# Kernel optimization log

Hardware: AMD Instinct MI355X
Metric: run time of the kernel (lower is better)

## Reference

```python
import jax, jax.numpy as jnp
import numpy as np

N = 100000      # nodes
E = 3200000     # edges
IN_DIM = 128
HID = 128
OUT_DIM = 1
LAYERS = 8
ALPHA = 0.1
THETA = 0.5


def setup_inputs() -> dict:
    key = jax.random.key(0)
    ks = jax.random.split(key, 8)
    x = jax.random.normal(ks[0], (N, IN_DIM), dtype=jnp.float32)
    edge_index = jax.random.randint(ks[1], (2, E), 0, N, dtype=jnp.int64)
    edge_weight = jax.random.uniform(ks[2], (E,), dtype=jnp.float32)  # unused by original forward path
    W_in = jax.random.normal(ks[3], (IN_DIM, HID), dtype=jnp.float32) * 0.05
    b_in = jnp.zeros((HID,), dtype=jnp.float32)
    W_gcn = jax.random.normal(ks[4], (LAYERS, HID, HID), dtype=jnp.float32) * 0.05
    W_out = jax.random.normal(ks[5], (HID, OUT_DIM), dtype=jnp.float32) * 0.05
    b_out = jnp.zeros((OUT_DIM,), dtype=jnp.float32)
    return {"x": x, "edge_weight": edge_weight, "W_in": W_in, "b_in": b_in,
            "W_gcn": W_gcn, "W_out": W_out, "b_out": b_out, "edge_index": edge_index}


def _gcn_norm(edge_index, dtype):
    # add self loops (fill value 1), symmetric normalization deg^-1/2 A deg^-1/2
    sl = jnp.arange(N, dtype=edge_index.dtype)
    row = jnp.concatenate([edge_index[0], sl])
    col = jnp.concatenate([edge_index[1], sl])
    w = jnp.ones(row.shape[0], dtype=dtype)
    deg = jax.ops.segment_sum(w, col, num_segments=N)
    dinv = jnp.where(deg > 0, jax.lax.rsqrt(deg), 0.0)
    norm = dinv[row] * dinv[col]
    return row, col, norm


def reference(x, edge_weight, W_in, b_in, W_gcn, W_out, b_out, edge_index):
    row, col, norm = _gcn_norm(edge_index, x.dtype)
    h = x @ W_in + b_in            # initial_proj
    h0 = h                          # residual x0
    for i in range(LAYERS):
        # dropout is identity in eval mode
        msg = h[row] * norm[:, None]                       # gather + scale [E+N, HID]
        agg = jax.ops.segment_sum(msg, col, num_segments=N)
        s = (1.0 - ALPHA) * agg + ALPHA * h0               # identity-mapped residual
        beta = float(np.log(THETA / (i + 1) + 1.0))
        h = (1.0 - beta) * s + beta * (s @ W_gcn[i])       # GCNII weight mix
        h = jax.nn.relu(h)
    return h @ W_out + b_out
```

## Files before the change

kernel.cpp:

```cpp
#include <hip/hip_runtime.h>
#include <hip/hip_bf16.h>
#include <math.h>

#define N_NODES 100000
#define N_EDGES 3200000
#define HID 128
#define LAYERS 8
#define ALPHA 0.1f
#define THETA 0.5f

#define SH 8
#define NODES8 (N_NODES * SH)
#define SCAN_TILE 4096
#define NB_SCAN ((NODES8 + SCAN_TILE - 1) / SCAN_TILE)

typedef unsigned int uint;
typedef unsigned short ushort;
typedef __attribute__((ext_vector_type(8))) short short8;
typedef __attribute__((ext_vector_type(4))) float f32x4;

__device__ inline float bf_lo(uint p) { return __uint_as_float(p << 16); }
__device__ inline float bf_hi(uint p) { return __uint_as_float(p & 0xffff0000u); }
__device__ inline uint bf_pack(float x, float y) {
    uint ux = __float_as_uint(x), uy = __float_as_uint(y);
    uint rx = (ux + 0x7fffu + ((ux >> 16) & 1u)) >> 16;
    uint ry = (uy + 0x7fffu + ((uy >> 16) & 1u)) >> 16;
    return rx | (ry << 16);
}
__device__ inline ushort bfr(float x) {
    uint u = __float_as_uint(x);
    return (ushort)((u + 0x7fffu + ((u >> 16) & 1u)) >> 16);
}
__device__ inline float bff(ushort s) { return __uint_as_float(((uint)s) << 16); }

__global__ __launch_bounds__(256) void k_count(const int* __restrict__ col,
                                               int* __restrict__ cnt8) {
    int e = blockIdx.x * 256 + threadIdx.x;
    int shard = blockIdx.x & (SH - 1);
    if (e < N_EDGES) atomicAdd(&cnt8[col[e] * SH + shard], 1);
}

__global__ __launch_bounds__(256) void k_dinv(const int* __restrict__ cnt8,
                                              float* __restrict__ dinv) {
    int n = blockIdx.x * 256 + threadIdx.x;
    if (n >= N_NODES) return;
    int4 a = *(const int4*)(cnt8 + n * SH);
    int4 b = *(const int4*)(cnt8 + n * SH + 4);
    int deg = a.x + a.y + a.z + a.w + b.x + b.y + b.z + b.w;
    dinv[n] = rsqrtf((float)(deg + 1));
}

__global__ __launch_bounds__(256) void k_scan1(const int* __restrict__ cnt8,
                                               int* __restrict__ indptr8,
                                               int* __restrict__ bsum) {
    __shared__ int lds[256];
    int t = threadIdx.x;
    int base = blockIdx.x * SCAN_TILE + t * 16;
    int v[16];
    int s = 0;
#pragma unroll
    for (int j = 0; j < 16; ++j) {
        v[j] = (base + j < NODES8) ? cnt8[base + j] : 0;
        s += v[j];
    }
    lds[t] = s;
    __syncthreads();
    for (int off = 1; off < 256; off <<= 1) {
        int u = (t >= off) ? lds[t - off] : 0;
        __syncthreads();
        lds[t] += u;
        __syncthreads();
    }
    int run = lds[t] - s;
#pragma unroll
    for (int j = 0; j < 16; ++j) {
        if (base + j < NODES8) indptr8[base + j] = run;
        run += v[j];
    }
    if (t == 255) bsum[blockIdx.x] = lds[255];
}

__global__ __launch_bounds__(256) void k_scan2(const int* __restrict__ bsum,
                                               int* __restrict__ boff) {
    __shared__ int lds[256];
    int t = threadIdx.x;
    int v = (t < NB_SCAN) ? bsum[t] : 0;
    lds[t] = v;
    __syncthreads();
    for (int off = 1; off < 256; off <<= 1) {
        int u = (t >= off) ? lds[t - off] : 0;
        __syncthreads();
        lds[t] += u;
        __syncthreads();
    }
    boff[t] = lds[t] - v;
}

__global__ __launch_bounds__(256) void k_scan3(int* __restrict__ indptr8,
                                               const int* __restrict__ boff) {
    int base = blockIdx.x * SCAN_TILE + threadIdx.x * 16;
    int add = boff[blockIdx.x];
#pragma unroll
    for (int j = 0; j < 16; ++j) {
        if (base + j < NODES8) indptr8[base + j] += add;
    }
    if (blockIdx.x == 0 && threadIdx.x == 0) indptr8[NODES8] = N_EDGES;
}

__global__ __launch_bounds__(256) void k_fill(const int* __restrict__ rowi,
                                              const int* __restrict__ coli,
                                              const float* __restrict__ dinv,
                                              const int* __restrict__ indptr8,
                                              int* __restrict__ cursor8,
                                              int2* __restrict__ csr) {
    int e = blockIdx.x * 256 + threadIdx.x;
    if (e >= N_EDGES) return;
    int shard = blockIdx.x & (SH - 1);
    int r = rowi[e];
    int c = coli[e];
    int slot = c * SH + shard;
    int p = indptr8[slot] + atomicAdd(&cursor8[slot], 1);
    csr[p] = make_int2(r, __float_as_int(dinv[r] * dinv[c]));
}

__global__ __launch_bounds__(256) void k_wprep(const float* __restrict__ Wg,
                                               ushort* __restrict__ Wt) {
    int l = blockIdx.x;
    const float* W = Wg + (size_t)l * HID * HID;
    ushort* T = Wt + (size_t)l * HID * HID;
    int t = threadIdx.x;
#pragma unroll
    for (int i = 0; i < 16; ++i) {
        int idx = t + 256 * i;
        int k = idx >> 5;
        int c4 = idx & 31;
        float4 v = *(const float4*)(W + (size_t)k * HID + c4 * 4);
        T[(c4 * 4 + 0) * HID + k] = bfr(v.x);
        T[(c4 * 4 + 1) * HID + k] = bfr(v.y);
        T[(c4 * 4 + 2) * HID + k] = bfr(v.z);
        T[(c4 * 4 + 3) * HID + k] = bfr(v.w);
    }
}

__global__ __launch_bounds__(256) void k_spmm(const uint* __restrict__ h,
                                              const uint* __restrict__ h0,
                                              const float* __restrict__ dinv,
                                              const int* __restrict__ indptr8,
                                              const int2* __restrict__ csr,
                                              uint* __restrict__ s_out) {
    int node = blockIdx.x * 4 + (threadIdx.x >> 6);
    if (node >= N_NODES) return;
    int lane = threadIdx.x & 63;
    int beg = indptr8[node * SH];
    int end = indptr8[node * SH + SH];
    float di = dinv[node];
    uint hs = h[node * 64 + lane];
    uint h0v = h0[node * 64 + lane];
    float ax[8], ay[8];
#pragma unroll
    for (int j = 0; j < 8; ++j) { ax[j] = 0.f; ay[j] = 0.f; }
    int e = beg;
    for (; e + 16 <= end; e += 16) {
        int2 rr[16];
#pragma unroll
        for (int j = 0; j < 16; ++j) rr[j] = csr[e + j];
        uint p[16];
#pragma unroll
        for (int j = 0; j < 16; ++j) p[j] = h[rr[j].x * 64 + lane];
#pragma unroll
        for (int j = 0; j < 16; ++j) {
            float w = __int_as_float(rr[j].y);
            ax[j & 7] = fmaf(w, bf_lo(p[j]), ax[j & 7]);
            ay[j & 7] = fmaf(w, bf_hi(p[j]), ay[j & 7]);
        }
    }
    for (; e < end; e += 4) {
        int2 rr[4];
        float w[4];
#pragma unroll
        for (int j = 0; j < 4; ++j) {
            int idx = e + j;
            rr[j] = csr[idx < end ? idx : beg];
            w[j] = (idx < end) ? __int_as_float(rr[j].y) : 0.f;
        }
        uint p[4];
#pragma unroll
        for (int j = 0; j < 4; ++j) p[j] = h[rr[j].x * 64 + lane];
#pragma unroll
        for (int j = 0; j < 4; ++j) {
            ax[j] = fmaf(w[j], bf_lo(p[j]), ax[j]);
            ay[j] = fmaf(w[j], bf_hi(p[j]), ay[j]);
        }
    }
    float sum0 = ((ax[0] + ax[1]) + (ax[2] + ax[3])) + ((ax[4] + ax[5]) + (ax[6] + ax[7]));
    float sum1 = ((ay[0] + ay[1]) + (ay[2] + ay[3])) + ((ay[4] + ay[5]) + (ay[6] + ay[7]));
    float selfw = di * di;
    float rx = (1.0f - ALPHA) * fmaf(selfw, bf_lo(hs), sum0) + ALPHA * bf_lo(h0v);
    float ry = (1.0f - ALPHA) * fmaf(selfw, bf_hi(hs), sum1) + ALPHA * bf_hi(h0v);
    s_out[node * 64 + lane] = bf_pack(rx, ry);
}

__global__ __launch_bounds__(256) void k_gemm_in(const float* __restrict__ A,
                                                 const float* __restrict__ W,
                                                 const float* __restrict__ bias,
                                                 uint* __restrict__ out0,
                                                 uint* __restrict__ out1) {
    __shared__ float sT[32 * 64];
    __shared__ float Ws[32 * 128];
    int t = threadIdx.x;
    int tr = t & 15;
    int tc = t >> 4;
    int rowBase = blockIdx.x * 64;
    float acc[4][8] = {};

    for (int ko = 0; ko < HID; ko += 32) {
#pragma unroll
        for (int pass = 0; pass < 2; ++pass) {
            int lin = t + 256 * pass;
            int r = lin >> 3;
            int kq = lin & 7;
            int ar = rowBase + r;
            if (ar >= N_NODES) ar = N_NODES - 1;
            float4 v = *(const float4*)(A + (size_t)ar * HID + ko + 4 * kq);
            sT[(4 * kq + 0) * 64 + r] = v.x;
            sT[(4 * kq + 1) * 64 + r] = v.y;
            sT[(4 * kq + 2) * 64 + r] = v.z;
            sT[(4 * kq + 3) * 64 + r] = v.w;
        }
#pragma unroll
        for (int pass = 0; pass < 4; ++pass) {
            int lin = t + 256 * pass;
            int k = lin >> 5;
            int c4 = lin & 31;
            *(float4*)&Ws[k * 128 + 4 * c4] =
                *(const float4*)(W + (size_t)(ko + k) * HID + 4 * c4);
        }
        __syncthreads();
#pragma unroll
        for (int k = 0; k < 32; ++k) {
            float4 a = *(const float4*)&sT[k * 64 + 4 * tr];
            float4 w0 = *(const float4*)&Ws[k * 128 + 8 * tc];
            float4 w1 = *(const float4*)&Ws[k * 128 + 8 * tc + 4];
            float av[4] = {a.x, a.y, a.z, a.w};
            float wv[8] = {w0.x, w0.y, w0.z, w0.w, w1.x, w1.y, w1.z, w1.w};
#pragma unroll
            for (int i = 0; i < 4; ++i)
#pragma unroll
                for (int j = 0; j < 8; ++j)
                    acc[i][j] = fmaf(av[i], wv[j], acc[i][j]);
        }
        __syncthreads();
    }

    int c0 = 8 * tc;
    float bb[8];
#pragma unroll
    for (int j = 0; j < 8; ++j) bb[j] = bias[c0 + j];
#pragma unroll
    for (int i = 0; i < 4; ++i) {
        int r = rowBase + 4 * tr + i;
        if (r >= N_NODES) break;
        float v[8];
#pragma unroll
        for (int j = 0; j < 8; ++j) v[j] = acc[i][j] + bb[j];
        uint4 o;
        o.x = bf_pack(v[0], v[1]);
        o.y = bf_pack(v[2], v[3]);
        o.z = bf_pack(v[4], v[5]);
        o.w = bf_pack(v[6], v[7]);
        *(uint4*)(out0 + (size_t)r * 64 + c0 / 2) = o;
        *(uint4*)(out1 + (size_t)r * 64 + c0 / 2) = o;
    }
}

#define SAS 136

__global__ __launch_bounds__(256) void k_gemm_layer(const uint* __restrict__ A,
                                                    const ushort* __restrict__ Wt,
                                                    uint* __restrict__ out0,
                                                    float beta) {
    __shared__ ushort sA[64 * SAS];
    __shared__ ushort sW[128 * SAS];
    int t = threadIdx.x;
    int lane = t & 63;
    int wv = t >> 6;
    int rowBase = blockIdx.x * 64;

#pragma unroll
    for (int i = 0; i < 4; ++i) {
        int idx = t + 256 * i;
        int r = idx >> 4;
        int q = idx & 15;
        int ar = rowBase + r;
        if (ar >= N_NODES) ar = N_NODES - 1;
        uint4 v = *(const uint4*)(A + (size_t)ar * 64 + q * 4);
        *(uint4*)((uint*)(sA + r * SAS) + q * 4) = v;
    }
#pragma unroll
    for (int i = 0; i < 8; ++i) {
        int idx = t + 256 * i;
        int r = idx >> 4;
        int q = idx & 15;
        uint4 v = *(const uint4*)((const uint*)(Wt + (size_t)r * HID) + q * 4);
        *(uint4*)((uint*)(sW + r * SAS) + q * 4) = v;
    }
    __syncthreads();

    int fr = lane & 15;
    int fq = lane >> 4;
    f32x4 acc[4][2] = {};
#pragma unroll
    for (int kc = 0; kc < 4; ++kc) {
        int kof = kc * 32 + fq * 8;
        short8 b0 = *(const short8*)(sW + (wv * 32 + fr) * SAS + kof);
        short8 b1 = *(const short8*)(sW + (wv * 32 + 16 + fr) * SAS + kof);
#pragma unroll
        for (int tm = 0; tm < 4; ++tm) {
            short8 a = *(const short8*)(sA + (tm * 16 + fr) * SAS + kof);
            acc[tm][0] = __builtin_amdgcn_mfma_f32_16x16x32_bf16(a, b0, acc[tm][0], 0, 0, 0);
            acc[tm][1] = __builtin_amdgcn_mfma_f32_16x16x32_bf16(a, b1, acc[tm][1], 0, 0, 0);
        }
    }
    __syncthreads();

    ushort* pack = sW;
    float ob = 1.0f - beta;
#pragma unroll
    for (int tm = 0; tm < 4; ++tm)
#pragma unroll
        for (int tn = 0; tn < 2; ++tn)
#pragma unroll
            for (int r = 0; r < 4; ++r) {
                int row = tm * 16 + fq * 4 + r;
                int col = wv * 32 + tn * 16 + fr;
                float sv = bff(sA[row * SAS + col]);
                float val = fmaxf(fmaf(ob, sv, beta * acc[tm][tn][r]), 0.f);
                pack[row * 128 + col] = bfr(val);
            }
    __syncthreads();
#pragma unroll
    for (int i = 0; i < 4; ++i) {
        int idx = t + 256 * i;
        int r = idx >> 4;
        int q = idx & 15;
        int ar = rowBase + r;
        if (ar < N_NODES)
            *(uint4*)(out0 + (size_t)ar * 64 + q * 4) =
                *(const uint4*)((const uint*)(pack + r * 128) + q * 4);
    }
}

__global__ __launch_bounds__(256) void k_out(const uint* __restrict__ h,
                                             const float* __restrict__ W_out,
                                             const float* __restrict__ b_out,
                                             float* __restrict__ out) {
    int node = blockIdx.x * 4 + (threadIdx.x >> 6);
    if (node >= N_NODES) return;
    int lane = threadIdx.x & 63;
    uint p = h[node * 64 + lane];
    float2 wv = *(const float2*)(W_out + lane * 2);
    float pr = bf_lo(p) * wv.x + bf_hi(p) * wv.y;
#pragma unroll
    for (int off = 32; off > 0; off >>= 1) pr += __shfl_down(pr, off);
    if (lane == 0) out[node] = pr + b_out[0];
}

extern "C" void kernel_launch(void* const* d_in, const int* in_sizes, int n_in,
                              void* d_out, int out_size, void* d_ws, size_t ws_size,
                              hipStream_t stream) {
    const float* x     = (const float*)d_in[0];
    const float* W_in  = (const float*)d_in[2];
    const float* b_in  = (const float*)d_in[3];
    const float* W_gcn = (const float*)d_in[4];
    const float* W_out = (const float*)d_in[5];
    const float* b_out = (const float*)d_in[6];
    const int*   ei    = (const int*)d_in[7];
    const int* rowi = ei;
    const int* coli = ei + N_EDGES;
    float* out = (float*)d_out;

    char* ws = (char*)d_ws;
    auto alloc = [&](size_t bytes) -> char* {
        char* p = ws;
        ws += (bytes + 255) & ~(size_t)255;
        return p;
    };
    int*    cnt8    = (int*)   alloc((size_t)NODES8 * 4);
    float*  dinv    = (float*) alloc((size_t)N_NODES * 4);
    int*    indptr8 = (int*)   alloc((size_t)(NODES8 + 8) * 4);
    int*    cursor8 = (int*)   alloc((size_t)NODES8 * 4);
    int*    bsum    = (int*)   alloc(1024 * 4);
    int*    boff    = (int*)   alloc(1024 * 4);
    int2*   csr     = (int2*)  alloc((size_t)N_EDGES * 8);
    ushort* Wt      = (ushort*)alloc((size_t)LAYERS * HID * HID * 2);
    uint*   hA      = (uint*)  alloc((size_t)N_NODES * 64 * 4);
    uint*   hB      = (uint*)  alloc((size_t)N_NODES * 64 * 4);
    uint*   h0      = (uint*)  alloc((size_t)N_NODES * 64 * 4);

    hipMemsetAsync(cnt8, 0, (size_t)NODES8 * 4, stream);
    hipMemsetAsync(cursor8, 0, (size_t)NODES8 * 4, stream);

    k_count<<<(N_EDGES + 255) / 256, 256, 0, stream>>>(coli, cnt8);
    k_dinv<<<(N_NODES + 255) / 256, 256, 0, stream>>>(cnt8, dinv);
    k_scan1<<<NB_SCAN, 256, 0, stream>>>(cnt8, indptr8, bsum);
    k_scan2<<<1, 256, 0, stream>>>(bsum, boff);
    k_scan3<<<NB_SCAN, 256, 0, stream>>>(indptr8, boff);
    k_fill<<<(N_EDGES + 255) / 256, 256, 0, stream>>>(rowi, coli, dinv, indptr8,
                                                      cursor8, csr);
    k_wprep<<<LAYERS, 256, 0, stream>>>(W_gcn, Wt);

    int gemm_blocks = (N_NODES + 63) / 64;
    k_gemm_in<<<gemm_blocks, 256, 0, stream>>>(x, W_in, b_in, h0, hA);

    for (int l = 0; l < LAYERS; ++l) {
        k_spmm<<<(N_NODES + 3) / 4, 256, 0, stream>>>(hA, h0, dinv, indptr8,
                                                      csr, hB);
        float beta = logf(THETA / (float)(l + 1) + 1.0f);
        k_gemm_layer<<<gemm_blocks, 256, 0, stream>>>(
            hB, Wt + (size_t)l * HID * HID, hA, beta);
    }
    k_out<<<(N_NODES + 3) / 4, 256, 0, stream>>>(hA, W_out, b_out, out);
}
```

Baseline: 1.533 ms.

## Build CSR via two-pass bucket binning with source-chunk sorted shards

Replaces the single atomic scatter CSR fill with a two-pass build: edges are first binned into 64-node destination buckets through coarse global atomics, then each bucket is scattered into CSR using shared-memory cursors. Shards are now keyed by source-node chunk rather than block index, so each node's neighbor list is grouped by source range, which is meant to improve gather locality in the SpMM layers. It targets the scattered global atomics and writes of the old fill, but adds an extra pass over the edges, a temp buffer and a single-block scan.

```diff
diff --git a/kernel.cpp b/kernel.cpp
--- a/kernel.cpp
+++ b/kernel.cpp
@@ -10,9 +10,14 @@
 #define THETA 0.5f
 
 #define SH 8
+#define CHDIV 12500
 #define NODES8 (N_NODES * SH)
 #define SCAN_TILE 4096
 #define NB_SCAN ((NODES8 + SCAN_TILE - 1) / SCAN_TILE)
+
+#define NBKT ((N_NODES + 63) / 64)
+#define NBKT8 (NBKT * 8)
+#define BPT 49
 
 typedef unsigned int uint;
 typedef unsigned short ushort;
@@ -33,11 +38,17 @@
 }
 __device__ inline float bff(ushort s) { return __uint_as_float(((uint)s) << 16); }
 
-__global__ __launch_bounds__(256) void k_count(const int* __restrict__ col,
-                                               int* __restrict__ cnt8) {
+__global__ __launch_bounds__(256) void k_count(const int* __restrict__ rowi,
+                                               const int* __restrict__ coli,
+                                               int* __restrict__ cnt8,
+                                               int* __restrict__ bktcnt8) {
     int e = blockIdx.x * 256 + threadIdx.x;
-    int shard = blockIdx.x & (SH - 1);
-    if (e < N_EDGES) atomicAdd(&cnt8[col[e] * SH + shard], 1);
+    if (e >= N_EDGES) return;
+    int r = rowi[e];
+    int c = coli[e];
+    int chunk = r / CHDIV;
+    atomicAdd(&cnt8[c * SH + chunk], 1);
+    atomicAdd(&bktcnt8[(c >> 6) * 8 + (blockIdx.x & 7)], 1);
 }
 
 __global__ __launch_bounds__(256) void k_dinv(const int* __restrict__ cnt8,
@@ -107,20 +118,78 @@
     if (blockIdx.x == 0 && threadIdx.x == 0) indptr8[NODES8] = N_EDGES;
 }
 
-__global__ __launch_bounds__(256) void k_fill(const int* __restrict__ rowi,
-                                              const int* __restrict__ coli,
-                                              const float* __restrict__ dinv,
-                                              const int* __restrict__ indptr8,
-                                              int* __restrict__ cursor8,
-                                              int2* __restrict__ csr) {
+__global__ __launch_bounds__(256) void k_bscan(const int* __restrict__ bktcnt8,
+                                               int* __restrict__ bktcur,
+                                               int* __restrict__ bktptr8) {
+    __shared__ int lds[256];
+    int t = threadIdx.x;
+    int base = t * BPT;
+    int v[BPT];
+    int s = 0;
+#pragma unroll
+    for (int j = 0; j < BPT; ++j) {
+        v[j] = (base + j < NBKT8) ? bktcnt8[base + j] : 0;
+        s += v[j];
+    }
+    lds[t] = s;
+    __syncthreads();
+    for (int off = 1; off < 256; off <<= 1) {
+        int u = (t >= off) ? lds[t - off] : 0;
+        __syncthreads();
+        lds[t] += u;
+        __syncthreads();
+    }
+    int run = lds[t] - s;
+#pragma unroll
+    for (int j = 0; j < BPT; ++j) {
+        if (base + j < NBKT8) { bktcur[base + j] = run; bktptr8[base + j] = run; }
+        run += v[j];
+    }
+    if (t == 255) bktptr8[NBKT8] = N_EDGES;
+}
+
+__global__ __launch_bounds__(256) void k_bin(const int* __restrict__ rowi,
+                                             const int* __restrict__ coli,
+                                             const float* __restrict__ dinv,
+                                             int* __restrict__ bktcur,
+                                             int2* __restrict__ binned) {
     int e = blockIdx.x * 256 + threadIdx.x;
     if (e >= N_EDGES) return;
-    int shard = blockIdx.x & (SH - 1);
     int r = rowi[e];
     int c = coli[e];
-    int slot = c * SH + shard;
-    int p = indptr8[slot] + atomicAdd(&cursor8[slot], 1);
-    csr[p] = make_int2(r, __float_as_int(dinv[r] * dinv[c]));
+    int chunk = r / CHDIV;
+    int stream = (c >> 6) * 8 + (blockIdx.x & 7);
+    int p = atomicAdd(&bktcur[stream], 1);
+    uint key = (uint)r | ((uint)(c & 63) << 17) | ((uint)chunk << 23);
+    binned[p] = make_int2((int)key, __float_as_int(dinv[r] * dinv[c]));
+}
+
+__global__ __launch_bounds__(256) void k_scatter(const int2* __restrict__ binned,
+                                                 const int* __restrict__ bktptr8,
+                                                 const int* __restrict__ indptr8,
+                                                 int2* __restrict__ csr) {
+    __shared__ int cur[512];
+    int b = blockIdx.x;
+    int t = threadIdx.x;
+    int nb = b * 64;
+#pragma unroll
+    for (int i = 0; i < 2; ++i) {
+        int idx = t + 256 * i;
+        int node = nb + (idx >> 3);
+        cur[idx] = (node < N_NODES) ? indptr8[node * SH + (idx & 7)] : 0;
+    }
+    __syncthreads();
+    int beg = bktptr8[b * 8];
+    int end = bktptr8[b * 8 + 8];
+    for (int i = beg + t; i < end; i += 256) {
+        int2 rec = binned[i];
+        uint key = (uint)rec.x;
+        int src = key & 0x1FFFF;
+        int coff = (key >> 17) & 63;
+        int chunk = (key >> 23) & 7;
+        int pos = atomicAdd(&cur[coff * 8 + chunk], 1);
+        csr[pos] = make_int2(src, rec.y);
+    }
 }
 
 __global__ __launch_bounds__(256) void k_wprep(const float* __restrict__ Wg,
@@ -388,9 +457,12 @@
     int*    cnt8    = (int*)   alloc((size_t)NODES8 * 4);
     float*  dinv    = (float*) alloc((size_t)N_NODES * 4);
     int*    indptr8 = (int*)   alloc((size_t)(NODES8 + 8) * 4);
-    int*    cursor8 = (int*)   alloc((size_t)NODES8 * 4);
+    int*    bktcnt8 = (int*)   alloc((size_t)NBKT8 * 4);
+    int*    bktcur  = (int*)   alloc((size_t)NBKT8 * 4);
+    int*    bktptr8 = (int*)   alloc((size_t)(NBKT8 + 8) * 4);
     int*    bsum    = (int*)   alloc(1024 * 4);
     int*    boff    = (int*)   alloc(1024 * 4);
+    int2*   binned  = (int2*)  alloc((size_t)N_EDGES * 8);
     int2*   csr     = (int2*)  alloc((size_t)N_EDGES * 8);
     ushort* Wt      = (ushort*)alloc((size_t)LAYERS * HID * HID * 2);
     uint*   hA      = (uint*)  alloc((size_t)N_NODES * 64 * 4);
@@ -398,15 +470,16 @@
     uint*   h0      = (uint*)  alloc((size_t)N_NODES * 64 * 4);
 
     hipMemsetAsync(cnt8, 0, (size_t)NODES8 * 4, stream);
-    hipMemsetAsync(cursor8, 0, (size_t)NODES8 * 4, stream);
-
-    k_count<<<(N_EDGES + 255) / 256, 256, 0, stream>>>(coli, cnt8);
+    hipMemsetAsync(bktcnt8, 0, (size_t)NBKT8 * 4, stream);
+
+    k_count<<<(N_EDGES + 255) / 256, 256, 0, stream>>>(rowi, coli, cnt8, bktcnt8);
     k_dinv<<<(N_NODES + 255) / 256, 256, 0, stream>>>(cnt8, dinv);
     k_scan1<<<NB_SCAN, 256, 0, stream>>>(cnt8, indptr8, bsum);
     k_scan2<<<1, 256, 0, stream>>>(bsum, boff);
     k_scan3<<<NB_SCAN, 256, 0, stream>>>(indptr8, boff);
-    k_fill<<<(N_EDGES + 255) / 256, 256, 0, stream>>>(rowi, coli, dinv, indptr8,
-                                                      cursor8, csr);
+    k_bscan<<<1, 256, 0, stream>>>(bktcnt8, bktcur, bktptr8);
+    k_bin<<<(N_EDGES + 255) / 256, 256, 0, stream>>>(rowi, coli, dinv, bktcur, binned);
+    k_scatter<<<NBKT, 256, 0, stream>>>(binned, bktptr8, indptr8, csr);
     k_wprep<<<LAYERS, 256, 0, stream>>>(W_gcn, Wt);
 
     int gemm_blocks = (N_NODES + 63) / 64;
```

Result: slower. 1.800 ms (+17.5%).
